# Kernel optimization log

Measured on AMD Instinct MI355X. Metric: run time of the kernel, lower is better.

Reference implementation:

```python
import jax, jax.numpy as jnp
import numpy as np
import math

B, C, L = 8, 64, 2048
H = 4            # num_heads
CH = C // H      # head channels = 16
G = max(1, C // 16)  # GroupNorm groups = 4
EPS = 1e-5


def setup_inputs() -> dict:
    key = jax.random.key(0)
    ks = jax.random.split(key, 4)
    x = jax.random.normal(ks[0], (B, C, L), dtype=jnp.float32)
    gn_w = jnp.ones((C,), jnp.float32)
    gn_b = jnp.zeros((C,), jnp.float32)
    qkv_w = jax.random.normal(ks[1], (3 * C, C), jnp.float32) / math.sqrt(C)
    qkv_b = jnp.zeros((3 * C,), jnp.float32)
    # note: original zero-inits proj_out; we use random weights for a non-trivial baseline
    proj_w = jax.random.normal(ks[2], (C, C), jnp.float32) / math.sqrt(C)
    proj_b = jnp.zeros((C,), jnp.float32)
    return {"x": x, "gn_w": gn_w, "gn_b": gn_b, "qkv_w": qkv_w,
            "qkv_b": qkv_b, "proj_w": proj_w, "proj_b": proj_b}


def _group_norm(x, w, b):
    # x: [B, C, L], groups over channel dim
    xg = x.reshape(B, G, (C // G) * L)
    mean = jnp.mean(xg, axis=-1, keepdims=True)
    var = jnp.var(xg, axis=-1, keepdims=True)
    xn = ((xg - mean) * jax.lax.rsqrt(var + EPS)).reshape(B, C, L)
    return xn * w[None, :, None] + b[None, :, None]


def reference(x, gn_w, gn_b, qkv_w, qkv_b, proj_w, proj_b):
    xn = _group_norm(x, gn_w, gn_b)
    # conv1x1 QKV: [B, 3C, L]
    qkv = jnp.einsum('oc,bcl->bol', qkv_w, xn) + qkv_b[None, :, None]
    q, k, v = jnp.split(qkv, 3, axis=1)            # each [B, C, L]
    q = q.reshape(B * H, CH, L)
    k = k.reshape(B * H, CH, L)
    v = v.reshape(B * H, CH, L)
    scale = 1.0 / math.sqrt(math.sqrt(CH))          # double-scaled as in source
    w = jnp.einsum('bct,bcs->bts', q * scale, k * scale)  # [B*H, L, L]
    w = jax.nn.softmax(w.astype(jnp.float32), axis=-1).astype(q.dtype)
    a = jnp.einsum('bts,bcs->bct', w, v).reshape(B, C, L)
    h = jnp.einsum('oc,bcl->bol', proj_w, a) + proj_b[None, :, None]
    return x + h
```

## Files before the change

### kernel.cpp

```cpp
#include <hip/hip_runtime.h>
#include <hip/hip_bf16.h>

#define LL 2048

typedef float f32x16 __attribute__((ext_vector_type(16)));
typedef float f32x4 __attribute__((ext_vector_type(4)));
typedef short short8 __attribute__((ext_vector_type(8)));

__device__ __forceinline__ float exp2_fast(float x) {
    float r;
    asm volatile("v_exp_f32 %0, %1" : "=v"(r) : "v"(x));
    return r;
}

__device__ __forceinline__ uint32_t pack2(float a, float b) {
    union { __hip_bfloat16 h; unsigned short s; } ua, ub;
    ua.h = __float2bfloat16(a);
    ub.h = __float2bfloat16(b);
    return (uint32_t)ua.s | ((uint32_t)ub.s << 16);
}

__device__ __forceinline__ unsigned short bf16of(float a) {
    union { __hip_bfloat16 h; unsigned short s; } u;
    u.h = __float2bfloat16(a);
    return u.s;
}

__device__ __forceinline__ void permswap(uint32_t& d, uint32_t& s) {
    asm("v_permlane32_swap_b32 %0, %1" : "+v"(d), "+v"(s));
}

__global__ __launch_bounds__(256) void k_gnstats(const float* __restrict__ x,
                                                 float* __restrict__ stats) {
    int bg = blockIdx.x >> 2, part = blockIdx.x & 3;
    const f32x4* p = (const f32x4*)(x + (size_t)bg * (16 * LL)) + part * 2048;
    float s1 = 0.f, s2 = 0.f;
    for (int i = threadIdx.x; i < 2048; i += 256) {
        f32x4 v = p[i];
        s1 += v[0] + v[1] + v[2] + v[3];
        s2 += v[0] * v[0] + v[1] * v[1] + v[2] * v[2] + v[3] * v[3];
    }
#pragma unroll
    for (int off = 32; off > 0; off >>= 1) {
        s1 += __shfl_down(s1, off, 64);
        s2 += __shfl_down(s2, off, 64);
    }
    __shared__ float r1[4], r2[4];
    int lane = threadIdx.x & 63, wv = threadIdx.x >> 6;
    if (lane == 0) { r1[wv] = s1; r2[wv] = s2; }
    __syncthreads();
    if (threadIdx.x == 0) {
        stats[blockIdx.x * 2]     = r1[0] + r1[1] + r1[2] + r1[3];
        stats[blockIdx.x * 2 + 1] = r2[0] + r2[1] + r2[2] + r2[3];
    }
}

__global__ __launch_bounds__(256) void k_qkv(const float* __restrict__ x,
                                             const float* __restrict__ gnw,
                                             const float* __restrict__ gnb,
                                             const float* __restrict__ qw,
                                             const float* __restrict__ qb,
                                             const float* __restrict__ stats,
                                             unsigned short* __restrict__ qt,
                                             unsigned short* __restrict__ kt,
                                             unsigned short* __restrict__ vb) {
    int lt = blockIdx.x;
    int ot = blockIdx.y;
    int b  = blockIdx.z;
    int tid = threadIdx.x;
    int l0 = lt * 64;
    __shared__ unsigned short xs[64 * 64];
    __shared__ unsigned short ws[64 * 64];

#pragma unroll
    for (int k = 0; k < 4; k++) {
        int chunk = tid + k * 256;
        int c = chunk >> 4, l4 = chunk & 15;
        f32x4 v = *(const f32x4*)(x + ((size_t)b * 64 + c) * LL + l0 + l4 * 4);
        int g = c >> 4;
        int sb = (b * 4 + g) * 8;
        float s1 = stats[sb] + stats[sb + 2] + stats[sb + 4] + stats[sb + 6];
        float s2 = stats[sb + 1] + stats[sb + 3] + stats[sb + 5] + stats[sb + 7];
        float mean = s1 * (1.0f / 32768.0f);
        float var  = s2 * (1.0f / 32768.0f) - mean * mean;
        float rstd = rsqrtf(var + 1e-5f);
        float wgt = gnw[c] * rstd;
        float bia = gnb[c] - mean * wgt;
#pragma unroll
        for (int j = 0; j < 4; j++) {
            int l = l4 * 4 + j;
            xs[l * 64 + (c ^ ((l & 7) << 3))] = bf16of(v[j] * wgt + bia);
        }
        int o = c, c4 = l4;
        f32x4 wv4 = *(const f32x4*)(qw + (size_t)(ot * 64 + o) * 64 + c4 * 4);
        uint2 pw2 = make_uint2(pack2(wv4[0], wv4[1]), pack2(wv4[2], wv4[3]));
        *(uint2*)&ws[o * 64 + ((c4 * 4) ^ ((o & 7) << 3))] = pw2;
    }
    __syncthreads();

    int wv_ = tid >> 6, lane = tid & 63, hi = lane >> 5, tl = lane & 31;
    int o0 = (wv_ & 1) * 32, lw = (wv_ >> 1) * 32;
    int arow = o0 + tl, brow = lw + tl;
    f32x16 acc = {};
#pragma unroll
    for (int kk = 0; kk < 4; kk++) {
        int cb = kk * 16 + hi * 8;
        short8 af = *(const short8*)&ws[arow * 64 + (cb ^ ((arow & 7) << 3))];
        short8 bf = *(const short8*)&xs[brow * 64 + (cb ^ ((brow & 7) << 3))];
        acc = __builtin_amdgcn_mfma_f32_32x32x16_bf16(af, bf, acc, 0, 0, 0);
    }

    int t = l0 + lw + tl;
    if (ot < 2) {
        float sc = ot ? 0.72134752f : 0.5f;
        unsigned short* base = (ot ? kt : qt) + (size_t)(b * 4) * (LL * 16);
#pragma unroll
        for (int g = 0; g < 4; g++) {
            int ob = o0 + 8 * g + 4 * hi;
            float v0 = (acc[4 * g]     + qb[ot * 64 + ob])     * sc;
            float v1 = (acc[4 * g + 1] + qb[ot * 64 + ob + 1]) * sc;
            float v2 = (acc[4 * g + 2] + qb[ot * 64 + ob + 2]) * sc;
            float v3 = (acc[4 * g + 3] + qb[ot * 64 + ob + 3]) * sc;
            uint2 pkv = make_uint2(pack2(v0, v1), pack2(v2, v3));
            *(uint2*)(base + (size_t)(ob >> 4) * (LL * 16) + (size_t)t * 16 + (ob & 15)) = pkv;
        }
    } else {
        unsigned short* base = vb + (size_t)(b * 4) * (16 * LL);
#pragma unroll
        for (int r = 0; r < 16; r++) {
            int o = o0 + (r & 3) + 8 * (r >> 2) + 4 * hi;
            base[(size_t)(o >> 4) * (16 * LL) + (size_t)(o & 15) * LL + t] =
                bf16of(acc[r] + qb[128 + o]);
        }
    }
}

__global__ __launch_bounds__(256) void k_attn(const unsigned short* __restrict__ qt,
                                              const unsigned short* __restrict__ kt,
                                              const unsigned short* __restrict__ vb,
                                              unsigned short* __restrict__ abuf) {
    int wv = threadIdx.x >> 6;
    int lane = threadIdx.x & 63;
    int hi = lane >> 5, tlo = lane & 31;
    int bh = blockIdx.y;
    int t0 = blockIdx.x * 32;

    __shared__ float lds_d2[3][32][17];
    __shared__ float lds_l[3][32];

    const unsigned short* qp = qt + (size_t)bh * (LL * 16);
    const unsigned short* kp = kt + (size_t)bh * (LL * 16);
    const unsigned short* vp = vb + (size_t)bh * (16 * LL) + (size_t)(tlo & 15) * LL;

    short8 qf = *(const short8*)(qp + (size_t)(t0 + tlo) * 16 + 8 * hi);

    f32x16 d2 = {};
    float lsum = 0.f;

    int sbeg = wv * 512;
    for (int s0 = sbeg; s0 < sbeg + 512; s0 += 32) {
        short8 kf  = *(const short8*)(kp + (size_t)(s0 + tlo) * 16 + 8 * hi);
        short8 vf0 = *(const short8*)(vp + s0 + 8 * hi);
        short8 vf1 = *(const short8*)(vp + s0 + 16 + 8 * hi);

        f32x16 z = {};
        f32x16 d1 = __builtin_amdgcn_mfma_f32_32x32x16_bf16(kf, qf, z, 0, 0, 0);

        float p[16], ps = 0.f;
#pragma unroll
        for (int r = 0; r < 16; r++) { p[r] = exp2_fast(d1[r]); ps += p[r]; }
        lsum += ps;

        uint32_t pk[8];
#pragma unroll
        for (int i = 0; i < 8; i++) pk[i] = pack2(p[2 * i], p[2 * i + 1]);

        permswap(pk[0], pk[2]);
        permswap(pk[1], pk[3]);
        permswap(pk[4], pk[6]);
        permswap(pk[5], pk[7]);
        union { uint32_t u[4]; short8 s; } A1, A2;
        A1.u[0] = pk[0]; A1.u[1] = pk[1]; A1.u[2] = pk[2]; A1.u[3] = pk[3];
        A2.u[0] = pk[4]; A2.u[1] = pk[5]; A2.u[2] = pk[6]; A2.u[3] = pk[7];

        d2 = __builtin_amdgcn_mfma_f32_32x32x16_bf16(A1.s, vf0, d2, 0, 0, 0);
        d2 = __builtin_amdgcn_mfma_f32_32x32x16_bf16(A2.s, vf1, d2, 0, 0, 0);
    }

    float ls = lsum + __shfl_xor(lsum, 32, 64);

    if (wv > 0) {
        int w = wv - 1;
#pragma unroll
        for (int r = 0; r < 16; r++) {
            int row = (r & 3) + 8 * (r >> 2) + 4 * hi;
            if (tlo < 16) lds_d2[w][row][tlo] = d2[r];
        }
        if (hi == 0) lds_l[w][tlo] = ls;
    }
    __syncthreads();
    if (wv == 0) {
        float lall = ls + lds_l[0][tlo] + lds_l[1][tlo] + lds_l[2][tlo];
        float rl = 1.0f / lall;
        int tc = tlo & 15;
        unsigned short* op = abuf + ((size_t)bh * 16 + tlo) * LL + t0;
        float v[16];
#pragma unroll
        for (int r = 0; r < 16; r++) {
            int row = (r & 3) + 8 * (r >> 2) + 4 * hi;
            float osum = d2[r] + lds_d2[0][row][tc]
                       + lds_d2[1][row][tc] + lds_d2[2][row][tc];
            v[r] = osum * __shfl(rl, row, 64);
        }
        if (tlo < 16) {
#pragma unroll
            for (int g = 0; g < 4; g++) {
                uint2 pkv = make_uint2(pack2(v[4 * g], v[4 * g + 1]),
                                       pack2(v[4 * g + 2], v[4 * g + 3]));
                *(uint2*)(op + 8 * g + 4 * hi) = pkv;
            }
        }
    }
}

__global__ __launch_bounds__(256) void k_proj(const float* __restrict__ x,
                                              const unsigned short* __restrict__ abuf,
                                              const float* __restrict__ pw,
                                              const float* __restrict__ pb,
                                              float* __restrict__ out) {
    int lt = blockIdx.x;
    int b  = blockIdx.y;
    int tid = threadIdx.x;
    int l0 = lt * 64;
    __shared__ unsigned short as_[64 * 64];
    __shared__ unsigned short ws[64 * 64];

#pragma unroll
    for (int k = 0; k < 2; k++) {
        int chunk = tid + k * 256;
        int c = chunk >> 3, l8 = chunk & 7;
        uint4 v8 = *(const uint4*)(abuf + (size_t)(b * 64 + c) * LL + l0 + l8 * 8);
        const unsigned short* sp = (const unsigned short*)&v8;
#pragma unroll
        for (int j = 0; j < 8; j++) {
            int l = l8 * 8 + j;
            as_[l * 64 + (c ^ ((l & 7) << 3))] = sp[j];
        }
    }
#pragma unroll
    for (int k = 0; k < 4; k++) {
        int chunk = tid + k * 256;
        int o = chunk >> 4, c4 = chunk & 15;
        f32x4 wv4 = *(const f32x4*)(pw + (size_t)o * 64 + c4 * 4);
        uint2 pw2 = make_uint2(pack2(wv4[0], wv4[1]), pack2(wv4[2], wv4[3]));
        *(uint2*)&ws[o * 64 + ((c4 * 4) ^ ((o & 7) << 3))] = pw2;
    }
    __syncthreads();

    int wv_ = tid >> 6, lane = tid & 63, hi = lane >> 5, tl = lane & 31;
    int o0 = (wv_ & 1) * 32, lw = (wv_ >> 1) * 32;
    int arow = o0 + tl, brow = lw + tl;
    f32x16 acc = {};
#pragma unroll
    for (int kk = 0; kk < 4; kk++) {
        int cb = kk * 16 + hi * 8;
        short8 af = *(const short8*)&ws[arow * 64 + (cb ^ ((arow & 7) << 3))];
        short8 bf = *(const short8*)&as_[brow * 64 + (cb ^ ((brow & 7) << 3))];
        acc = __builtin_amdgcn_mfma_f32_32x32x16_bf16(af, bf, acc, 0, 0, 0);
    }

    int l = l0 + lw + tl;
#pragma unroll
    for (int r = 0; r < 16; r++) {
        int o = o0 + (r & 3) + 8 * (r >> 2) + 4 * hi;
        size_t idx = (size_t)(b * 64 + o) * LL + l;
        out[idx] = x[idx] + acc[r] + pb[o];
    }
}

extern "C" void kernel_launch(void* const* d_in, const int* in_sizes, int n_in,
                              void* d_out, int out_size, void* d_ws, size_t ws_size,
                              hipStream_t stream) {
    const float* x   = (const float*)d_in[0];
    const float* gnw = (const float*)d_in[1];
    const float* gnb = (const float*)d_in[2];
    const float* qw  = (const float*)d_in[3];
    const float* qb  = (const float*)d_in[4];
    const float* pw  = (const float*)d_in[5];
    const float* pb  = (const float*)d_in[6];
    float* out = (float*)d_out;

    float* wsf   = (float*)d_ws;
    float* stats = wsf;
    unsigned short* qt = (unsigned short*)(wsf + 256);
    unsigned short* kt = qt + (size_t)32 * LL * 16;
    unsigned short* vb = kt + (size_t)32 * LL * 16;
    unsigned short* abuf = vb + (size_t)32 * LL * 16;

    hipLaunchKernelGGL(k_gnstats, dim3(128), dim3(256), 0, stream, x, stats);
    hipLaunchKernelGGL(k_qkv, dim3(32, 3, 8), dim3(256), 0, stream,
                       x, gnw, gnb, qw, qb, stats, qt, kt, vb);
    hipLaunchKernelGGL(k_attn, dim3(64, 32), dim3(256), 0, stream, qt, kt, vb, abuf);
    hipLaunchKernelGGL(k_proj, dim3(32, 8), dim3(256), 0, stream,
                       x, abuf, pw, pb, out);
}
```

Baseline: 124.9 us.

## Fold softmax row sums into MFMA via ones column; prefetch K/V; vectorize LDS staging

In the attention kernel the idle upper 16 columns of the P·V MFMA are fed a buffer of bf16 ones, so the softmax denominator comes out of the matrix unit. This removes the per-element VALU summation and the separate lds_l reduction, and the normalization is then taken through a lane shuffle. The K/V fragment loads are software-prefetched one iteration ahead. The QKV and projection kernels restage their LDS writes as 4-channel packed 64-bit stores with per-channel GN scale and bias precomputed in shared memory. The denominator now sums bf16-rounded probabilities, and the ones buffer needs extra workspace written by the stats kernel.

```diff
diff --git a/kernel.cpp b/kernel.cpp
--- a/kernel.cpp
+++ b/kernel.cpp
@@ -31,7 +31,13 @@
 }
 
 __global__ __launch_bounds__(256) void k_gnstats(const float* __restrict__ x,
-                                                 float* __restrict__ stats) {
+                                                 float* __restrict__ stats,
+                                                 unsigned short* __restrict__ ones) {
+    if (blockIdx.x == 0) {
+        uint4 v = make_uint4(0x3F803F80u, 0x3F803F80u, 0x3F803F80u, 0x3F803F80u);
+        *(uint4*)(ones + threadIdx.x * 16)     = v;
+        *(uint4*)(ones + threadIdx.x * 16 + 8) = v;
+    }
     int bg = blockIdx.x >> 2, part = blockIdx.x & 3;
     const f32x4* p = (const f32x4*)(x + (size_t)bg * (16 * LL)) + part * 2048;
     float s1 = 0.f, s2 = 0.f;
@@ -71,13 +77,10 @@
     int l0 = lt * 64;
     __shared__ unsigned short xs[64 * 64];
     __shared__ unsigned short ws[64 * 64];
-
-#pragma unroll
-    for (int k = 0; k < 4; k++) {
-        int chunk = tid + k * 256;
-        int c = chunk >> 4, l4 = chunk & 15;
-        f32x4 v = *(const f32x4*)(x + ((size_t)b * 64 + c) * LL + l0 + l4 * 4);
-        int g = c >> 4;
+    __shared__ float wb[64][2];
+
+    if (tid < 64) {
+        int c = tid, g = c >> 4;
         int sb = (b * 4 + g) * 8;
         float s1 = stats[sb] + stats[sb + 2] + stats[sb + 4] + stats[sb + 6];
         float s2 = stats[sb + 1] + stats[sb + 3] + stats[sb + 5] + stats[sb + 7];
@@ -85,16 +88,36 @@
         float var  = s2 * (1.0f / 32768.0f) - mean * mean;
         float rstd = rsqrtf(var + 1e-5f);
         float wgt = gnw[c] * rstd;
-        float bia = gnb[c] - mean * wgt;
-#pragma unroll
-        for (int j = 0; j < 4; j++) {
-            int l = l4 * 4 + j;
-            xs[l * 64 + (c ^ ((l & 7) << 3))] = bf16of(v[j] * wgt + bia);
-        }
-        int o = c, c4 = l4;
+        wb[c][0] = wgt;
+        wb[c][1] = gnb[c] - mean * wgt;
+    }
+#pragma unroll
+    for (int k = 0; k < 4; k++) {
+        int chunk = tid + k * 256;
+        int o = chunk >> 4, c4 = chunk & 15;
         f32x4 wv4 = *(const f32x4*)(qw + (size_t)(ot * 64 + o) * 64 + c4 * 4);
         uint2 pw2 = make_uint2(pack2(wv4[0], wv4[1]), pack2(wv4[2], wv4[3]));
         *(uint2*)&ws[o * 64 + ((c4 * 4) ^ ((o & 7) << 3))] = pw2;
+    }
+    __syncthreads();
+
+    {
+        int cq = tid >> 4, l4 = tid & 15, c0 = cq * 4;
+        f32x4 xv0 = *(const f32x4*)(x + ((size_t)b * 64 + c0)     * LL + l0 + l4 * 4);
+        f32x4 xv1 = *(const f32x4*)(x + ((size_t)b * 64 + c0 + 1) * LL + l0 + l4 * 4);
+        f32x4 xv2 = *(const f32x4*)(x + ((size_t)b * 64 + c0 + 2) * LL + l0 + l4 * 4);
+        f32x4 xv3 = *(const f32x4*)(x + ((size_t)b * 64 + c0 + 3) * LL + l0 + l4 * 4);
+        float w0 = wb[c0][0], b0 = wb[c0][1];
+        float w1 = wb[c0 + 1][0], b1 = wb[c0 + 1][1];
+        float w2 = wb[c0 + 2][0], b2 = wb[c0 + 2][1];
+        float w3 = wb[c0 + 3][0], b3 = wb[c0 + 3][1];
+#pragma unroll
+        for (int j = 0; j < 4; j++) {
+            int l = l4 * 4 + j;
+            uint32_t lo = pack2(xv0[j] * w0 + b0, xv1[j] * w1 + b1);
+            uint32_t hw = pack2(xv2[j] * w2 + b2, xv3[j] * w3 + b3);
+            *(uint2*)&xs[l * 64 + (c0 ^ ((l & 7) << 3))] = make_uint2(lo, hw);
+        }
     }
     __syncthreads();
 
@@ -138,6 +161,7 @@
 __global__ __launch_bounds__(256) void k_attn(const unsigned short* __restrict__ qt,
                                               const unsigned short* __restrict__ kt,
                                               const unsigned short* __restrict__ vb,
+                                              const unsigned short* __restrict__ ones,
                                               unsigned short* __restrict__ abuf) {
     int wv = threadIdx.x >> 6;
     int lane = threadIdx.x & 63;
@@ -145,31 +169,35 @@
     int bh = blockIdx.y;
     int t0 = blockIdx.x * 32;
 
-    __shared__ float lds_d2[3][32][17];
-    __shared__ float lds_l[3][32];
+    __shared__ float lds_d2[3][32][33];
 
     const unsigned short* qp = qt + (size_t)bh * (LL * 16);
     const unsigned short* kp = kt + (size_t)bh * (LL * 16);
-    const unsigned short* vp = vb + (size_t)bh * (16 * LL) + (size_t)(tlo & 15) * LL;
+    const unsigned short* vp = (tlo < 16)
+        ? vb + (size_t)bh * (16 * LL) + (size_t)tlo * LL
+        : ones;
 
     short8 qf = *(const short8*)(qp + (size_t)(t0 + tlo) * 16 + 8 * hi);
 
     f32x16 d2 = {};
-    float lsum = 0.f;
-
-    int sbeg = wv * 512;
-    for (int s0 = sbeg; s0 < sbeg + 512; s0 += 32) {
-        short8 kf  = *(const short8*)(kp + (size_t)(s0 + tlo) * 16 + 8 * hi);
-        short8 vf0 = *(const short8*)(vp + s0 + 8 * hi);
-        short8 vf1 = *(const short8*)(vp + s0 + 16 + 8 * hi);
+
+    int sbeg = wv * 512, send = sbeg + 512;
+    short8 kf  = *(const short8*)(kp + (size_t)(sbeg + tlo) * 16 + 8 * hi);
+    short8 vf0 = *(const short8*)(vp + sbeg + 8 * hi);
+    short8 vf1 = *(const short8*)(vp + sbeg + 16 + 8 * hi);
+
+    for (int s0 = sbeg; s0 < send; s0 += 32) {
+        int sn = (s0 + 32 < send) ? s0 + 32 : sbeg;
+        short8 kn  = *(const short8*)(kp + (size_t)(sn + tlo) * 16 + 8 * hi);
+        short8 vn0 = *(const short8*)(vp + sn + 8 * hi);
+        short8 vn1 = *(const short8*)(vp + sn + 16 + 8 * hi);
 
         f32x16 z = {};
         f32x16 d1 = __builtin_amdgcn_mfma_f32_32x32x16_bf16(kf, qf, z, 0, 0, 0);
 
-        float p[16], ps = 0.f;
-#pragma unroll
-        for (int r = 0; r < 16; r++) { p[r] = exp2_fast(d1[r]); ps += p[r]; }
-        lsum += ps;
+        float p[16];
+#pragma unroll
+        for (int r = 0; r < 16; r++) p[r] = exp2_fast(d1[r]);
 
         uint32_t pk[8];
 #pragma unroll
@@ -185,32 +213,30 @@
 
         d2 = __builtin_amdgcn_mfma_f32_32x32x16_bf16(A1.s, vf0, d2, 0, 0, 0);
         d2 = __builtin_amdgcn_mfma_f32_32x32x16_bf16(A2.s, vf1, d2, 0, 0, 0);
-    }
-
-    float ls = lsum + __shfl_xor(lsum, 32, 64);
+
+        kf = kn; vf0 = vn0; vf1 = vn1;
+    }
 
     if (wv > 0) {
         int w = wv - 1;
 #pragma unroll
         for (int r = 0; r < 16; r++) {
             int row = (r & 3) + 8 * (r >> 2) + 4 * hi;
-            if (tlo < 16) lds_d2[w][row][tlo] = d2[r];
-        }
-        if (hi == 0) lds_l[w][tlo] = ls;
+            lds_d2[w][row][tlo] = d2[r];
+        }
     }
     __syncthreads();
     if (wv == 0) {
-        float lall = ls + lds_l[0][tlo] + lds_l[1][tlo] + lds_l[2][tlo];
-        float rl = 1.0f / lall;
-        int tc = tlo & 15;
         unsigned short* op = abuf + ((size_t)bh * 16 + tlo) * LL + t0;
         float v[16];
 #pragma unroll
         for (int r = 0; r < 16; r++) {
             int row = (r & 3) + 8 * (r >> 2) + 4 * hi;
-            float osum = d2[r] + lds_d2[0][row][tc]
-                       + lds_d2[1][row][tc] + lds_d2[2][row][tc];
-            v[r] = osum * __shfl(rl, row, 64);
+            float osum = d2[r] + lds_d2[0][row][tlo]
+                       + lds_d2[1][row][tlo] + lds_d2[2][row][tlo];
+            float rv = 1.0f / osum;
+            float rl = __shfl_xor(rv, 16, 64);
+            v[r] = osum * rl;
         }
         if (tlo < 16) {
 #pragma unroll
@@ -235,16 +261,22 @@
     __shared__ unsigned short as_[64 * 64];
     __shared__ unsigned short ws[64 * 64];
 
-#pragma unroll
-    for (int k = 0; k < 2; k++) {
-        int chunk = tid + k * 256;
-        int c = chunk >> 3, l8 = chunk & 7;
-        uint4 v8 = *(const uint4*)(abuf + (size_t)(b * 64 + c) * LL + l0 + l8 * 8);
-        const unsigned short* sp = (const unsigned short*)&v8;
-#pragma unroll
-        for (int j = 0; j < 8; j++) {
-            int l = l8 * 8 + j;
-            as_[l * 64 + (c ^ ((l & 7) << 3))] = sp[j];
+    {
+        int cq = tid >> 4, t4 = tid & 15, c0 = cq * 4;
+        uint2 ld0 = *(const uint2*)(abuf + (size_t)(b * 64 + c0)     * LL + l0 + t4 * 4);
+        uint2 ld1 = *(const uint2*)(abuf + (size_t)(b * 64 + c0 + 1) * LL + l0 + t4 * 4);
+        uint2 ld2 = *(const uint2*)(abuf + (size_t)(b * 64 + c0 + 2) * LL + l0 + t4 * 4);
+        uint2 ld3 = *(const uint2*)(abuf + (size_t)(b * 64 + c0 + 3) * LL + l0 + t4 * 4);
+        const unsigned short* s0 = (const unsigned short*)&ld0;
+        const unsigned short* s1 = (const unsigned short*)&ld1;
+        const unsigned short* s2 = (const unsigned short*)&ld2;
+        const unsigned short* s3 = (const unsigned short*)&ld3;
+#pragma unroll
+        for (int j = 0; j < 4; j++) {
+            int l = t4 * 4 + j;
+            uint32_t lo = (uint32_t)s0[j] | ((uint32_t)s1[j] << 16);
+            uint32_t hw = (uint32_t)s2[j] | ((uint32_t)s3[j] << 16);
+            *(uint2*)&as_[l * 64 + (c0 ^ ((l & 7) << 3))] = make_uint2(lo, hw);
         }
     }
 #pragma unroll
@@ -296,11 +328,13 @@
     unsigned short* kt = qt + (size_t)32 * LL * 16;
     unsigned short* vb = kt + (size_t)32 * LL * 16;
     unsigned short* abuf = vb + (size_t)32 * LL * 16;
-
-    hipLaunchKernelGGL(k_gnstats, dim3(128), dim3(256), 0, stream, x, stats);
+    unsigned short* ones = abuf + (size_t)8 * 64 * LL;
+
+    hipLaunchKernelGGL(k_gnstats, dim3(128), dim3(256), 0, stream, x, stats, ones);
     hipLaunchKernelGGL(k_qkv, dim3(32, 3, 8), dim3(256), 0, stream,
                        x, gnw, gnb, qw, qb, stats, qt, kt, vb);
-    hipLaunchKernelGGL(k_attn, dim3(64, 32), dim3(256), 0, stream, qt, kt, vb, abuf);
+    hipLaunchKernelGGL(k_attn, dim3(64, 32), dim3(256), 0, stream,
+                       qt, kt, vb, ones, abuf);
     hipLaunchKernelGGL(k_proj, dim3(32, 8), dim3(256), 0, stream,
                        x, abuf, pw, pb, out);
 }
```

Result: faster. 121.2 us (-2.9%).
